# Kernel optimization log

Measured on AMD Instinct MI355X. Metric: run time of the kernel, lower is better.

## Reference

```python
import jax, jax.numpy as jnp
from jax import lax
import numpy as np

PADDING = 1
STRIDE = 1


def setup_inputs() -> dict:
    key = jax.random.key(0)
    k1, k2 = jax.random.split(key)
    x = jax.random.normal(k1, (256, 224, 224), dtype=jnp.float32)       # [C, H, W]
    kernel = jax.random.normal(k2, (256, 256, 3, 3), dtype=jnp.float32)  # [O, C, kh, kw]
    return {"x": x, "kernel": kernel}


def reference(x, kernel):
    # Direct conv2d with zero padding and stride, equivalent to the
    # nested-loop torch implementation (cross-correlation, no bias).
    out = lax.conv_general_dilated(
        x[None],                      # [1, C, H, W]
        kernel,                       # [O, C, kh, kw]
        window_strides=(STRIDE, STRIDE),
        padding=[(PADDING, PADDING), (PADDING, PADDING)],
        dimension_numbers=("NCHW", "OIHW", "NCHW"),
    )
    return out[0]                     # [O, Hout, Wout]
```

## Files before the change

### kernel.cpp

```cpp
#include <hip/hip_runtime.h>
#include <hip/hip_bf16.h>
#include <stdint.h>

#define C_IN  256
#define C_OUT 256
#define H_IN  224
#define W_IN  224
#define HP    226
#define WP    226
#define NPIX  (H_IN * W_IN)
#define BM    128
#define BN    128
#define BK    64

typedef __attribute__((ext_vector_type(8))) short short8;
typedef __attribute__((ext_vector_type(4))) float f32x4;

__device__ __forceinline__ unsigned short f2bf(float f) {
    __hip_bfloat16 b = __float2bfloat16(f);
    return *(unsigned short*)&b;
}

__device__ __forceinline__ void gl_lds16(const unsigned short* g, unsigned short* l) {
    __builtin_amdgcn_global_load_lds(
        (const __attribute__((address_space(1))) unsigned int*)g,
        (__attribute__((address_space(3))) unsigned int*)l,
        16, 0, 0);
}


__global__ void prep_misc(const float* __restrict__ wk, unsigned short* __restrict__ wb,
                          unsigned short* __restrict__ xp) {
    int b = blockIdx.x;
    if (b < 2304) {
        int idx = b * 256 + threadIdx.x;
        int c = idx & 255, o = (idx >> 8) & 255, p = idx >> 16;
        wb[((size_t)p * 256 + o) * 256 + c] = f2bf(wk[((size_t)o * 256 + c) * 9 + p]);
        return;
    }
    int i = (b - 2304) * 256 + threadIdx.x;
    uint4 z = make_uint4(0u, 0u, 0u, 0u);
    if (i < 7232) {
        ((uint4*)xp)[i] = z;
    } else if (i < 14464) {
        ((uint4*)(xp + (size_t)225 * WP * C_IN))[i - 7232] = z;
    } else if (i < 21632) {
        int j = i - 14464; int h = 1 + (j >> 5); int c4 = j & 31;
        ((uint4*)(xp + ((size_t)h * WP) * C_IN))[c4] = z;
    } else if (i < 28800) {
        int j = i - 21632; int h = 1 + (j >> 5); int c4 = j & 31;
        ((uint4*)(xp + ((size_t)h * WP + 225) * C_IN))[c4] = z;
    }
}

__global__ void prep_x(const float* __restrict__ x, unsigned short* __restrict__ xp) {
    int b  = blockIdx.x;
    int ct = b & 3, wt = (b >> 2) & 3, h = b >> 4;
    int c0 = ct * 64, w0 = wt * 64;
    int t  = threadIdx.x;
    __shared__ float tile[64][65];

    int w   = t & 63;
    int cl0 = t >> 6;
    #pragma unroll
    for (int i = 0; i < 16; ++i) {
        int cl = i * 4 + cl0;
        float v = 0.f;
        if (w0 + w < W_IN)
            v = x[(size_t)(c0 + cl) * NPIX + (size_t)h * W_IN + w0 + w];
        tile[cl][w] = v;
    }
    __syncthreads();

    int wc = t >> 2;
    int cc = (t & 3) * 16;
    if (w0 + wc < W_IN) {
        uint32_t pk[8];
        #pragma unroll
        for (int j = 0; j < 8; ++j) {
            unsigned short lo = f2bf(tile[cc + 2 * j][wc]);
            unsigned short hi = f2bf(tile[cc + 2 * j + 1][wc]);
            pk[j] = (uint32_t)lo | ((uint32_t)hi << 16);
        }
        size_t base = ((size_t)(h + 1) * WP + (w0 + wc + 1)) * C_IN + c0 + cc;
        uint4* dst = (uint4*)(xp + base);
        dst[0] = make_uint4(pk[0], pk[1], pk[2], pk[3]);
        dst[1] = make_uint4(pk[4], pk[5], pk[6], pk[7]);
    }
}


__launch_bounds__(256, 2)
__global__ void conv_gemm(const unsigned short* __restrict__ xp,
                          const unsigned short* __restrict__ wb,
                          float* __restrict__ out) {
    int wgid = (blockIdx.x & 7) * 98 + (blockIdx.x >> 3);
    int mt = wgid & 1;
    int nt = wgid >> 1;
    int m0 = mt * BM;
    int n0 = nt * BN;
    int t  = threadIdx.x;
    int l  = t & 63, wv = t >> 6;

    __shared__ __align__(16) unsigned short lds[2 * 16384];

    int q8 = ((l & 7) ^ (l >> 3)) * 8;
    int rA = l >> 3;
    int offA0, offA1, offA2, offA3, offB0, offB1, offB2, offB3;
    {
        int r0 = (wv * 4 + 0) * 8 + rA;
        int r1 = (wv * 4 + 1) * 8 + rA;
        int r2 = (wv * 4 + 2) * 8 + rA;
        int r3 = (wv * 4 + 3) * 8 + rA;
        offA0 = (m0 + r0) * C_IN + q8;
        offA1 = (m0 + r1) * C_IN + q8;
        offA2 = (m0 + r2) * C_IN + q8;
        offA3 = (m0 + r3) * C_IN + q8;
        int nc0 = n0 + r0, nc1 = n0 + r1, nc2 = n0 + r2, nc3 = n0 + r3;
        int h0 = nc0 / W_IN, h1 = nc1 / W_IN, h2 = nc2 / W_IN, h3 = nc3 / W_IN;
        offB0 = (h0 * WP + (nc0 - h0 * W_IN)) * C_IN + q8;
        offB1 = (h1 * WP + (nc1 - h1 * W_IN)) * C_IN + q8;
        offB2 = (h2 * WP + (nc2 - h2 * W_IN)) * C_IN + q8;
        offB3 = (h3 * WP + (nc3 - h3 * W_IN)) * C_IN + q8;
    }

    int la = l & 15;
    int lk = l >> 4;
    int mo = (wv >> 1) * 64;
    int no = (wv & 1) * 64;
    int xq0 = ((0 * 4 + lk) ^ (la & 7)) * 8;
    int xq1 = ((1 * 4 + lk) ^ (la & 7)) * 8;

    f32x4 acc[4][4];
    #pragma unroll
    for (int i = 0; i < 4; ++i)
        #pragma unroll
        for (int j = 0; j < 4; ++j)
            acc[i][j] = f32x4{0.f, 0.f, 0.f, 0.f};

#define STAGE(BD, S) do {                                                    \
    int s_ = (S);                                                            \
    int p_ = s_ >> 2, cs_ = (s_ & 3) << 6;                                   \
    int kh_ = (p_ * 11) >> 5; int kw_ = p_ - 3 * kh_;                        \
    const unsigned short* aS_ = wb + p_ * 65536 + cs_;                       \
    const unsigned short* bS_ = xp + (kh_ * WP + kw_) * C_IN + cs_;          \
    gl_lds16(aS_ + offA0, &lds[(BD) * 16384 + (wv * 4 + 0) * 512]);          \
    gl_lds16(aS_ + offA1, &lds[(BD) * 16384 + (wv * 4 + 1) * 512]);          \
    gl_lds16(aS_ + offA2, &lds[(BD) * 16384 + (wv * 4 + 2) * 512]);          \
    gl_lds16(aS_ + offA3, &lds[(BD) * 16384 + (wv * 4 + 3) * 512]);          \
    gl_lds16(bS_ + offB0, &lds[(BD) * 16384 + 8192 + (wv * 4 + 0) * 512]);   \
    gl_lds16(bS_ + offB1, &lds[(BD) * 16384 + 8192 + (wv * 4 + 1) * 512]);   \
    gl_lds16(bS_ + offB2, &lds[(BD) * 16384 + 8192 + (wv * 4 + 2) * 512]);   \
    gl_lds16(bS_ + offB3, &lds[(BD) * 16384 + 8192 + (wv * 4 + 3) * 512]);   \
} while (0)

#define MFMA16(AF, BF) do {                                                  \
    __builtin_amdgcn_s_setprio(1);                                           \
    _Pragma("unroll")                                                        \
    for (int i_ = 0; i_ < 4; ++i_)                                           \
        _Pragma("unroll")                                                    \
        for (int j_ = 0; j_ < 4; ++j_)                                       \
            acc[i_][j_] = __builtin_amdgcn_mfma_f32_16x16x32_bf16(           \
                AF[i_], BF[j_], acc[i_][j_], 0, 0, 0);                       \
    __builtin_amdgcn_s_setprio(0);                                           \
} while (0)

#define LGKM0() do {                                                         \
    asm volatile("s_waitcnt lgkmcnt(0)" ::: "memory");                       \
    __builtin_amdgcn_sched_barrier(0);                                       \
} while (0)

#define BODY(BC, S, DO_STAGE) do {                                           \
    asm volatile("s_waitcnt vmcnt(0)" ::: "memory");                         \
    __builtin_amdgcn_sched_barrier(0);                                       \
    __builtin_amdgcn_s_barrier();                                            \
    __builtin_amdgcn_sched_barrier(0);                                       \
    short8 a0_[4], b0_[4], a1_[4], b1_[4];                                   \
    _Pragma("unroll")                                                        \
    for (int i_ = 0; i_ < 4; ++i_) {                                         \
        a0_[i_] = *(const short8*)&lds[(BC) * 16384 + (mo + i_ * 16 + la) * BK + xq0]; \
        b0_[i_] = *(const short8*)&lds[(BC) * 16384 + 8192 + (no + i_ * 16 + la) * BK + xq0]; \
    }                                                                        \
    if (DO_STAGE) STAGE((BC) ^ 1, (S) + 1);                                  \
    LGKM0();                                                                 \
    MFMA16(a0_, b0_);                                                        \
    _Pragma("unroll")                                                        \
    for (int i_ = 0; i_ < 4; ++i_) {                                         \
        a1_[i_] = *(const short8*)&lds[(BC) * 16384 + (mo + i_ * 16 + la) * BK + xq1]; \
        b1_[i_] = *(const short8*)&lds[(BC) * 16384 + 8192 + (no + i_ * 16 + la) * BK + xq1]; \
    }                                                                        \
    LGKM0();                                                                 \
    MFMA16(a1_, b1_);                                                        \
    __builtin_amdgcn_sched_barrier(0);                                       \
    __builtin_amdgcn_s_barrier();                                            \
    __builtin_amdgcn_sched_barrier(0);                                       \
} while (0)

    STAGE(0, 0);
    #pragma unroll 1
    for (int k = 0; k < 17; ++k) {
        BODY(0, 2 * k, 1);
        BODY(1, 2 * k + 1, 1);
    }
    BODY(0, 34, 1);
    BODY(1, 35, 0);

#undef BODY
#undef LGKM0
#undef MFMA16
#undef STAGE

    int ro = lk * 4;
    #pragma unroll
    for (int i = 0; i < 4; ++i) {
        #pragma unroll
        for (int j = 0; j < 4; ++j) {
            int oo = m0 + mo + i * 16 + ro;
            int nn = n0 + no + j * 16 + la;
            #pragma unroll
            for (int r = 0; r < 4; ++r)
                out[(size_t)(oo + r) * NPIX + nn] = acc[i][j][r];
        }
    }
}

__global__ void conv_naive(const float* __restrict__ x, const float* __restrict__ wk,
                           float* __restrict__ out) {
    int idx = blockIdx.x * 256 + threadIdx.x;
    int n = idx % NPIX;
    int o = idx / NPIX;
    int h = n / W_IN, w = n - (n / W_IN) * W_IN;
    float s = 0.f;
    for (int c = 0; c < C_IN; ++c) {
        const float* xc = x + (size_t)c * NPIX;
        const float* wc = wk + ((size_t)o * C_IN + c) * 9;
        #pragma unroll
        for (int kh = 0; kh < 3; ++kh) {
            int hh = h + kh - 1;
            if (hh < 0 || hh >= H_IN) continue;
            #pragma unroll
            for (int kw = 0; kw < 3; ++kw) {
                int ww = w + kw - 1;
                if (ww < 0 || ww >= W_IN) continue;
                s += xc[hh * W_IN + ww] * wc[kh * 3 + kw];
            }
        }
    }
    out[idx] = s;
}

extern "C" void kernel_launch(void* const* d_in, const int* in_sizes, int n_in,
                              void* d_out, int out_size, void* d_ws, size_t ws_size,
                              hipStream_t stream) {
    const float* x  = (const float*)d_in[0];
    const float* wk = (const float*)d_in[1];
    float* out = (float*)d_out;

    const size_t xp_elems = (size_t)HP * WP * C_IN;
    const size_t wb_elems = (size_t)9 * 256 * 256;
    const size_t need = (xp_elems + wb_elems) * 2;

    if (ws_size < need) {
        conv_naive<<<(C_OUT * NPIX) / 256, 256, 0, stream>>>(x, wk, out);
        return;
    }

    unsigned short* xp = (unsigned short*)d_ws;
    unsigned short* wb = xp + xp_elems;

    prep_misc<<<2304 + 113, 256, 0, stream>>>(wk, wb, xp);
    prep_x<<<224 * 16, 256, 0, stream>>>(x, xp);
    conv_gemm<<<392 * 2, 256, 0, stream>>>(xp, wb, out);
}
```

Baseline: 95.15 us.

## Load weight fragments directly from global into registers, halving LDS footprint

The A-operand (weight) tiles are no longer staged through LDS. Each wave now loads its MFMA fragments straight from global memory into registers every K step, while only the im2col input tile is double-buffered in LDS. This halves shared memory per block, which together with launch_bounds raised to 3 blocks per CU is meant to increase occupancy and cut LDS read traffic. In exchange, A loads are issued synchronously within each iteration rather than one stage ahead, so their global latency may be exposed, and the register budget tightens.

```diff
diff --git a/kernel.cpp b/kernel.cpp
--- a/kernel.cpp
+++ b/kernel.cpp
@@ -90,7 +90,7 @@
 }
 
 
-__launch_bounds__(256, 2)
+__launch_bounds__(256, 3)
 __global__ void conv_gemm(const unsigned short* __restrict__ xp,
                           const unsigned short* __restrict__ wb,
                           float* __restrict__ out) {
@@ -102,20 +102,16 @@
     int t  = threadIdx.x;
     int l  = t & 63, wv = t >> 6;
 
-    __shared__ __align__(16) unsigned short lds[2 * 16384];
+    __shared__ __align__(16) unsigned short lds[2 * 8192];
 
     int q8 = ((l & 7) ^ (l >> 3)) * 8;
     int rA = l >> 3;
-    int offA0, offA1, offA2, offA3, offB0, offB1, offB2, offB3;
+    int offB0, offB1, offB2, offB3;
     {
         int r0 = (wv * 4 + 0) * 8 + rA;
         int r1 = (wv * 4 + 1) * 8 + rA;
         int r2 = (wv * 4 + 2) * 8 + rA;
         int r3 = (wv * 4 + 3) * 8 + rA;
-        offA0 = (m0 + r0) * C_IN + q8;
-        offA1 = (m0 + r1) * C_IN + q8;
-        offA2 = (m0 + r2) * C_IN + q8;
-        offA3 = (m0 + r3) * C_IN + q8;
         int nc0 = n0 + r0, nc1 = n0 + r1, nc2 = n0 + r2, nc3 = n0 + r3;
         int h0 = nc0 / W_IN, h1 = nc1 / W_IN, h2 = nc2 / W_IN, h3 = nc3 / W_IN;
         offB0 = (h0 * WP + (nc0 - h0 * W_IN)) * C_IN + q8;
@@ -130,6 +126,7 @@
     int no = (wv & 1) * 64;
     int xq0 = ((0 * 4 + lk) ^ (la & 7)) * 8;
     int xq1 = ((1 * 4 + lk) ^ (la & 7)) * 8;
+    int aRow = (m0 + mo + la) * C_IN + lk * 8;
 
     f32x4 acc[4][4];
     #pragma unroll
@@ -138,65 +135,64 @@
         for (int j = 0; j < 4; ++j)
             acc[i][j] = f32x4{0.f, 0.f, 0.f, 0.f};
 
-#define STAGE(BD, S) do {                                                    \
+    short8 aR[4][2];
+
+#define STAGE_B(BD, S) do {                                                  \
     int s_ = (S);                                                            \
     int p_ = s_ >> 2, cs_ = (s_ & 3) << 6;                                   \
     int kh_ = (p_ * 11) >> 5; int kw_ = p_ - 3 * kh_;                        \
-    const unsigned short* aS_ = wb + p_ * 65536 + cs_;                       \
     const unsigned short* bS_ = xp + (kh_ * WP + kw_) * C_IN + cs_;          \
-    gl_lds16(aS_ + offA0, &lds[(BD) * 16384 + (wv * 4 + 0) * 512]);          \
-    gl_lds16(aS_ + offA1, &lds[(BD) * 16384 + (wv * 4 + 1) * 512]);          \
-    gl_lds16(aS_ + offA2, &lds[(BD) * 16384 + (wv * 4 + 2) * 512]);          \
-    gl_lds16(aS_ + offA3, &lds[(BD) * 16384 + (wv * 4 + 3) * 512]);          \
-    gl_lds16(bS_ + offB0, &lds[(BD) * 16384 + 8192 + (wv * 4 + 0) * 512]);   \
-    gl_lds16(bS_ + offB1, &lds[(BD) * 16384 + 8192 + (wv * 4 + 1) * 512]);   \
-    gl_lds16(bS_ + offB2, &lds[(BD) * 16384 + 8192 + (wv * 4 + 2) * 512]);   \
-    gl_lds16(bS_ + offB3, &lds[(BD) * 16384 + 8192 + (wv * 4 + 3) * 512]);   \
+    gl_lds16(bS_ + offB0, &lds[(BD) * 8192 + (wv * 4 + 0) * 512]);           \
+    gl_lds16(bS_ + offB1, &lds[(BD) * 8192 + (wv * 4 + 1) * 512]);           \
+    gl_lds16(bS_ + offB2, &lds[(BD) * 8192 + (wv * 4 + 2) * 512]);           \
+    gl_lds16(bS_ + offB3, &lds[(BD) * 8192 + (wv * 4 + 3) * 512]);           \
 } while (0)
 
-#define MFMA16(AF, BF) do {                                                  \
+#define LOAD_A(S) do {                                                       \
+    int s_ = (S);                                                            \
+    const unsigned short* aS_ = wb + (s_ >> 2) * 65536 + ((s_ & 3) << 6) + aRow; \
+    _Pragma("unroll")                                                        \
+    for (int i_ = 0; i_ < 4; ++i_) {                                         \
+        aR[i_][0] = *(const short8*)(aS_ + i_ * 16 * C_IN);                  \
+        aR[i_][1] = *(const short8*)(aS_ + i_ * 16 * C_IN + 32);             \
+    }                                                                        \
+} while (0)
+
+#define BODY(BC, S, DO_STAGE) do {                                           \
+    LOAD_A(S);                                                               \
+    if (DO_STAGE) STAGE_B((BC) ^ 1, (S) + 1);                                \
+    asm volatile("s_waitcnt vmcnt(%0)" :: "i"((DO_STAGE) ? 4 : 0) : "memory"); \
+    __builtin_amdgcn_sched_barrier(0);                                       \
+    __builtin_amdgcn_s_barrier();                                            \
+    __builtin_amdgcn_sched_barrier(0);                                       \
+    short8 b0_[4], b1_[4];                                                   \
+    _Pragma("unroll")                                                        \
+    for (int i_ = 0; i_ < 4; ++i_) {                                         \
+        b0_[i_] = *(const short8*)&lds[(BC) * 8192 + (no + i_ * 16 + la) * BK + xq0]; \
+        b1_[i_] = *(const short8*)&lds[(BC) * 8192 + (no + i_ * 16 + la) * BK + xq1]; \
+    }                                                                        \
+    asm volatile("s_waitcnt lgkmcnt(0)" ::: "memory");                       \
+    __builtin_amdgcn_sched_barrier(0);                                       \
     __builtin_amdgcn_s_setprio(1);                                           \
     _Pragma("unroll")                                                        \
     for (int i_ = 0; i_ < 4; ++i_)                                           \
         _Pragma("unroll")                                                    \
         for (int j_ = 0; j_ < 4; ++j_)                                       \
             acc[i_][j_] = __builtin_amdgcn_mfma_f32_16x16x32_bf16(           \
-                AF[i_], BF[j_], acc[i_][j_], 0, 0, 0);                       \
+                aR[i_][0], b0_[j_], acc[i_][j_], 0, 0, 0);                   \
+    _Pragma("unroll")                                                        \
+    for (int i_ = 0; i_ < 4; ++i_)                                           \
+        _Pragma("unroll")                                                    \
+        for (int j_ = 0; j_ < 4; ++j_)                                       \
+            acc[i_][j_] = __builtin_amdgcn_mfma_f32_16x16x32_bf16(           \
+                aR[i_][1], b1_[j_], acc[i_][j_], 0, 0, 0);                   \
     __builtin_amdgcn_s_setprio(0);                                           \
+    __builtin_amdgcn_sched_barrier(0);                                       \
+    __builtin_amdgcn_s_barrier();                                            \
+    __builtin_amdgcn_sched_barrier(0);                                       \
 } while (0)
 
-#define LGKM0() do {                                                         \
-    asm volatile("s_waitcnt lgkmcnt(0)" ::: "memory");                       \
-    __builtin_amdgcn_sched_barrier(0);                                       \
-} while (0)
-
-#define BODY(BC, S, DO_STAGE) do {                                           \
-    asm volatile("s_waitcnt vmcnt(0)" ::: "memory");                         \
-    __builtin_amdgcn_sched_barrier(0);                                       \
-    __builtin_amdgcn_s_barrier();                                            \
-    __builtin_amdgcn_sched_barrier(0);                                       \
-    short8 a0_[4], b0_[4], a1_[4], b1_[4];                                   \
-    _Pragma("unroll")                                                        \
-    for (int i_ = 0; i_ < 4; ++i_) {                                         \
-        a0_[i_] = *(const short8*)&lds[(BC) * 16384 + (mo + i_ * 16 + la) * BK + xq0]; \
-        b0_[i_] = *(const short8*)&lds[(BC) * 16384 + 8192 + (no + i_ * 16 + la) * BK + xq0]; \
-    }                                                                        \
-    if (DO_STAGE) STAGE((BC) ^ 1, (S) + 1);                                  \
-    LGKM0();                                                                 \
-    MFMA16(a0_, b0_);                                                        \
-    _Pragma("unroll")                                                        \
-    for (int i_ = 0; i_ < 4; ++i_) {                                         \
-        a1_[i_] = *(const short8*)&lds[(BC) * 16384 + (mo + i_ * 16 + la) * BK + xq1]; \
-        b1_[i_] = *(const short8*)&lds[(BC) * 16384 + 8192 + (no + i_ * 16 + la) * BK + xq1]; \
-    }                                                                        \
-    LGKM0();                                                                 \
-    MFMA16(a1_, b1_);                                                        \
-    __builtin_amdgcn_sched_barrier(0);                                       \
-    __builtin_amdgcn_s_barrier();                                            \
-    __builtin_amdgcn_sched_barrier(0);                                       \
-} while (0)
-
-    STAGE(0, 0);
+    STAGE_B(0, 0);
     #pragma unroll 1
     for (int k = 0; k < 17; ++k) {
         BODY(0, 2 * k, 1);
@@ -206,9 +202,8 @@
     BODY(1, 35, 0);
 
 #undef BODY
-#undef LGKM0
-#undef MFMA16
-#undef STAGE
+#undef LOAD_A
+#undef STAGE_B
 
     int ro = lk * 4;
     #pragma unroll
```

After: 183.6 us. +92.9%, slower.
